# Performance work log

Hardware: AMD Instinct MI355X
Metric: run time of the kernel (lower is better)

The kernel has to match this reference:

```python
import jax, jax.numpy as jnp
import numpy as np

T, DIM, HID = 8192, 1024, 4096

def setup_inputs() -> dict:
    key = jax.random.key(0)
    k1, k2, k3 = jax.random.split(key, 3)
    x = jax.random.normal(k1, (T, DIM), dtype=jnp.float32)
    # torch Linear weight layout: [out_features, in_features]
    W_fc = jax.random.normal(k2, (HID, DIM), dtype=jnp.float32) * 0.02
    W_proj = jax.random.normal(k3, (DIM, HID), dtype=jnp.float32) * 0.02
    return {"x": x, "W_fc": W_fc, "W_proj": W_proj}

def reference(x, W_fc, W_proj):
    # fc: x @ W_fc^T  -> relu -> square -> proj: @ W_proj^T
    h = jnp.einsum('td,hd->th', x, W_fc)      # [T, HID]
    h = jnp.square(jax.nn.relu(h))            # relu(h)^2 (relu^2 activation)
    return jnp.einsum('th,dh->td', h, W_proj) # [T, DIM]
```

## Files before the change

### kernel.cpp

```cpp
#include <hip/hip_runtime.h>
#include <stdint.h>


typedef __attribute__((ext_vector_type(8))) short bf16x8;
typedef __attribute__((ext_vector_type(4))) float f32x4;

typedef const __attribute__((address_space(1))) unsigned int* gas_u32p;
typedef __attribute__((address_space(3))) unsigned int* las_u32p;

__device__ __forceinline__ void load16_to_lds(const void* gptr, void* lptr) {
    __builtin_amdgcn_global_load_lds((gas_u32p)gptr, (las_u32p)lptr, 16, 0, 0);
}

__device__ __forceinline__ unsigned short f2bf(float f) {
    unsigned int u = __float_as_uint(f);
    u += 0x7FFFu + ((u >> 16) & 1u);
    return (unsigned short)(u >> 16);
}

__global__ void cvt_all(const float4* __restrict__ x,  ushort4* __restrict__ xb,
                        const float4* __restrict__ wf, ushort4* __restrict__ wfb,
                        const float4* __restrict__ wp, ushort4* __restrict__ wpb)
{
    const int base = blockIdx.x * 1024 + threadIdx.x;
    #pragma unroll
    for (int j = 0; j < 4; j++) {
        const int i = base + j * 256;
        const float4* s; ushort4* d; int k;
        if (i < (1 << 21))            { s = x;  d = xb;  k = i; }
        else if (i < 3 * (1 << 20))   { s = wf; d = wfb; k = i - (1 << 21); }
        else                          { s = wp; d = wpb; k = i - 3 * (1 << 20); }
        float4 v = s[k];
        ushort4 o;
        o.x = f2bf(v.x); o.y = f2bf(v.y); o.z = f2bf(v.z); o.w = f2bf(v.w);
        d[k] = o;
    }
}

#define LGKM0_FENCE() do { \
    asm volatile("s_waitcnt lgkmcnt(0)" ::: "memory"); \
    __builtin_amdgcn_sched_barrier(0); } while (0)

template<int NF, bool RELU2, bool OUT_BF16>
__global__ __launch_bounds__(512, 2)
void gemm8p(const unsigned short* __restrict__ A,
            const unsigned short* __restrict__ B,
            void* __restrict__ Cv, int M, int N, int K)
{
    constexpr int BM   = 256;
    constexpr int BN   = 64 * NF;
    constexpr int CB   = BN / 128;
    constexpr int AKH  = 16384;
    constexpr int BKH  = BN * 64;
    constexpr int BOFF = 2 * AKH;
    constexpr int BUFB = 2 * AKH + 2 * BKH;
    constexpr int KEEP = 2 + 2 * CB;
    (void)M;

    __shared__ char lds[2 * BUFB];

    const int tid  = threadIdx.x;
    const int lane = tid & 63;
    const int wave = tid >> 6;
    const int wm   = wave >> 2;
    const int wn   = wave & 3;
    const int quad = lane >> 4;
    const int m16  = lane & 15;

    const int gx = gridDim.x;
    int flat = blockIdx.y * gx + blockIdx.x;
    const int cpx = (gx * gridDim.y) >> 3;
    flat = (flat & 7) * cpx + (flat >> 3);
    const long bm0 = (long)(flat / gx) * BM;
    const long bn0 = (long)(flat % gx) * BN;

    const int srow   = tid >> 2;
    const int schunk = (tid & 3) ^ ((tid >> 3) & 3);
    const unsigned short* gA = A + (bm0 + srow) * (long)K + schunk * 8;
    const unsigned short* gB = B + (bn0 + srow) * (long)K + schunk * 8;
    char* lbase = (char*)lds;

    int offA[8], offB[NF];
    #pragma unroll
    for (int i = 0; i < 8; i++) {
        const int lo = (wm * 128 + i * 16 + m16) * 64 + quad * 16;
        offA[i] = lo ^ (((lo >> 7) & 3) << 4);
    }
    #pragma unroll
    for (int j = 0; j < NF; j++) {
        const int lo = (wn * 16 * NF + j * 16 + m16) * 64 + quad * 16;
        offB[j] = lo ^ (((lo >> 7) & 3) << 4);
    }

    f32x4 acc[8][NF];
    #pragma unroll
    for (int i = 0; i < 8; i++)
        #pragma unroll
        for (int j = 0; j < NF; j++)
            acc[i][j] = (f32x4)0.0f;

    const int NT = K >> 6;

    #define STAGE_A(t, kh) do { \
        char* _d = lbase + ((t) & 1) * BUFB + (kh) * AKH + tid * 16; \
        const unsigned short* _s = gA + (long)(t) * 64 + (kh) * 32; \
        load16_to_lds(_s, _d); \
        load16_to_lds(_s + 128l * K, _d + 8192); } while (0)

    #define STAGE_B(t, kh) do { \
        char* _d = lbase + ((t) & 1) * BUFB + BOFF + (kh) * BKH + tid * 16; \
        const unsigned short* _s = gB + (long)(t) * 64 + (kh) * 32; \
        load16_to_lds(_s, _d); \
        if (CB == 2) load16_to_lds(_s + 128l * K, _d + 8192); } while (0)

    STAGE_B(0, 0); STAGE_A(0, 0); STAGE_B(0, 1); STAGE_A(0, 1);
    if (NT > 1) {
        STAGE_B(1, 0); STAGE_A(1, 0); STAGE_B(1, 1);
        asm volatile("s_waitcnt vmcnt(%0)" :: "i"(KEEP) : "memory");
    } else {
        asm volatile("s_waitcnt vmcnt(0)" ::: "memory");
    }
    __builtin_amdgcn_sched_barrier(0);
    __builtin_amdgcn_s_barrier();

    for (int t = 0; t < NT; ++t) {
        char* bufA = lbase + (t & 1) * BUFB;
        char* bufB = bufA + BOFF;
        bf16x8 af[4], bf[NF];

        #pragma unroll
        for (int j = 0; j < NF; j++) bf[j] = *(const bf16x8*)(bufB + offB[j]);
        #pragma unroll
        for (int i = 0; i < 4; i++)  af[i] = *(const bf16x8*)(bufA + offA[i]);
        if (t + 1 < NT) STAGE_A(t + 1, 1);
        __builtin_amdgcn_s_barrier();
        LGKM0_FENCE();
        __builtin_amdgcn_s_setprio(1);
        #pragma unroll
        for (int i = 0; i < 4; i++)
            #pragma unroll
            for (int j = 0; j < NF; j++)
                acc[i][j] = __builtin_amdgcn_mfma_f32_16x16x32_bf16(
                    af[i], bf[j], acc[i][j], 0, 0, 0);
        __builtin_amdgcn_s_setprio(0);
        __builtin_amdgcn_s_barrier();

        #pragma unroll
        for (int i = 0; i < 4; i++)  af[i] = *(const bf16x8*)(bufA + offA[4 + i]);
        if (t + 2 < NT) STAGE_B(t + 2, 0);
        __builtin_amdgcn_s_barrier();
        LGKM0_FENCE();
        __builtin_amdgcn_s_setprio(1);
        #pragma unroll
        for (int i = 0; i < 4; i++)
            #pragma unroll
            for (int j = 0; j < NF; j++)
                acc[4 + i][j] = __builtin_amdgcn_mfma_f32_16x16x32_bf16(
                    af[i], bf[j], acc[4 + i][j], 0, 0, 0);
        __builtin_amdgcn_s_setprio(0);
        __builtin_amdgcn_s_barrier();

        #pragma unroll
        for (int j = 0; j < NF; j++) bf[j] = *(const bf16x8*)(bufB + BKH + offB[j]);
        #pragma unroll
        for (int i = 0; i < 4; i++)  af[i] = *(const bf16x8*)(bufA + AKH + offA[i]);
        if (t + 2 < NT) STAGE_A(t + 2, 0);
        __builtin_amdgcn_s_barrier();
        LGKM0_FENCE();
        __builtin_amdgcn_s_setprio(1);
        #pragma unroll
        for (int i = 0; i < 4; i++)
            #pragma unroll
            for (int j = 0; j < NF; j++)
                acc[i][j] = __builtin_amdgcn_mfma_f32_16x16x32_bf16(
                    af[i], bf[j], acc[i][j], 0, 0, 0);
        __builtin_amdgcn_s_setprio(0);
        __builtin_amdgcn_s_barrier();

        #pragma unroll
        for (int i = 0; i < 4; i++)  af[i] = *(const bf16x8*)(bufA + AKH + offA[4 + i]);
        if (t + 2 < NT) STAGE_B(t + 2, 1);
        __builtin_amdgcn_s_barrier();
        LGKM0_FENCE();
        __builtin_amdgcn_s_setprio(1);
        #pragma unroll
        for (int i = 0; i < 4; i++)
            #pragma unroll
            for (int j = 0; j < NF; j++)
                acc[4 + i][j] = __builtin_amdgcn_mfma_f32_16x16x32_bf16(
                    af[i], bf[j], acc[4 + i][j], 0, 0, 0);
        __builtin_amdgcn_s_setprio(0);
        if (t + 2 < NT) asm volatile("s_waitcnt vmcnt(%0)" :: "i"(KEEP) : "memory");
        else            asm volatile("s_waitcnt vmcnt(0)" ::: "memory");
        __builtin_amdgcn_sched_barrier(0);
        __builtin_amdgcn_s_barrier();
    }
    #undef STAGE_A
    #undef STAGE_B

    const long baseRow = bm0 + wm * 128 + quad * 4;
    const long baseCol = bn0 + wn * 16 * NF + m16;
    #pragma unroll
    for (int i = 0; i < 8; i++) {
        #pragma unroll
        for (int j = 0; j < NF; j++) {
            #pragma unroll
            for (int r = 0; r < 4; r++) {
                float v = acc[i][j][r];
                if (RELU2) v = (v > 0.0f) ? v * v : 0.0f;
                const long row = baseRow + i * 16 + r;
                const long col = baseCol + j * 16;
                if (OUT_BF16)
                    ((unsigned short*)Cv)[row * (long)N + col] = f2bf(v);
                else
                    ((float*)Cv)[row * (long)N + col] = v;
            }
        }
    }
}

extern "C" void kernel_launch(void* const* d_in, const int* in_sizes, int n_in,
                              void* d_out, int out_size, void* d_ws, size_t ws_size,
                              hipStream_t stream) {
    (void)in_sizes; (void)n_in; (void)out_size; (void)ws_size;

    const int T = 8192, DIM = 1024, HID = 4096;

    const float* x     = (const float*)d_in[0];
    const float* W_fc  = (const float*)d_in[1];
    const float* W_prj = (const float*)d_in[2];
    float* out = (float*)d_out;

    char* ws = (char*)d_ws;
    unsigned short* h   = (unsigned short*)ws;
    unsigned short* xb  = (unsigned short*)(ws + (64l << 20));
    unsigned short* wfb = (unsigned short*)(ws + (80l << 20));
    unsigned short* wpb = (unsigned short*)(ws + (88l << 20));

    cvt_all<<<4096, 256, 0, stream>>>(
        (const float4*)x,     (ushort4*)xb,
        (const float4*)W_fc,  (ushort4*)wfb,
        (const float4*)W_prj, (ushort4*)wpb);

    gemm8p<4, true, true><<<dim3(HID / 256, T / 256), dim3(512), 0, stream>>>(
        xb, wfb, h, T, HID, DIM);

    gemm8p<2, false, false><<<dim3(DIM / 128, T / 256), dim3(512), 0, stream>>>(
        h, wpb, out, T, DIM, HID);
}
```

Baseline: 244.9 us.

## Add skewed half-K pipelined GEMM kernel for projection with XCD-aware block remap

Replaces the second GEMM (h @ W_proj^T) with a new kernel that splits each 64-wide K tile into two halves, issuing async global-to-LDS loads for later halves while MFMAs run on earlier ones, with explicit waitcnt, barriers and setprio control. Block indices are remapped across 8 groups so that neighbouring tiles land on the same XCD. LDS reads use inline ds_read_b128 with XOR swizzle. It aims to hide load latency and improve L2 locality, at the cost of hand-tuned wait counts that are fragile and tied to the K tiling.

```diff
diff --git a/kernel.cpp b/kernel.cpp
--- a/kernel.cpp
+++ b/kernel.cpp
@@ -10,6 +10,10 @@
 
 __device__ __forceinline__ void load16_to_lds(const void* gptr, void* lptr) {
     __builtin_amdgcn_global_load_lds((gas_u32p)gptr, (las_u32p)lptr, 16, 0, 0);
+}
+
+__device__ __forceinline__ void dsr128(bf16x8& d, unsigned off) {
+    asm volatile("ds_read_b128 %0, %1" : "=v"(d) : "v"(off));
 }
 
 __device__ __forceinline__ unsigned short f2bf(float f) {
@@ -219,6 +223,141 @@
     }
 }
 
+__global__ __launch_bounds__(512, 2)
+void gemm_skew(const unsigned short* __restrict__ A,
+               const unsigned short* __restrict__ B,
+               float* __restrict__ C, int M, int N, int K)
+{
+    constexpr int AKH  = 16384;
+    constexpr int BKH  = 8192;
+    constexpr int BOFF = 2 * AKH;
+    constexpr int BUFB = 2 * AKH + 2 * BKH;
+    (void)M;
+
+    __shared__ char lds[2 * BUFB];
+
+    const int tid  = threadIdx.x;
+    const int lane = tid & 63;
+    const int wave = tid >> 6;
+    const int wm   = wave >> 1;
+    const int wn   = wave & 1;
+    const int quad = lane >> 4;
+    const int m16  = lane & 15;
+
+    const int gx = gridDim.x;
+    int flat = blockIdx.y * gx + blockIdx.x;
+    const int cpx = (gx * gridDim.y) >> 3;
+    flat = (flat & 7) * cpx + (flat >> 3);
+    const long bm0 = (long)(flat / gx) * 256;
+    const long bn0 = (long)(flat % gx) * 128;
+
+    const int srow   = tid >> 2;
+    const int schunk = (tid & 3) ^ ((tid >> 3) & 3);
+    const unsigned short* gA = A + (bm0 + srow) * (long)K + schunk * 8;
+    const unsigned short* gB = B + (bn0 + srow) * (long)K + schunk * 8;
+
+    unsigned offA[4], offB[4];
+    #pragma unroll
+    for (int i = 0; i < 4; i++) {
+        const unsigned lo = (unsigned)((wm * 64 + i * 16 + m16) * 64 + quad * 16);
+        offA[i] = lo ^ (((lo >> 7) & 3) << 4);
+    }
+    #pragma unroll
+    for (int j = 0; j < 4; j++) {
+        const unsigned lo = (unsigned)((wn * 64 + j * 16 + m16) * 64 + quad * 16);
+        offB[j] = lo ^ (((lo >> 7) & 3) << 4);
+    }
+
+    const unsigned ldsbase =
+        (unsigned)(unsigned long long)(las_u32p)(void*)lds;
+
+    f32x4 acc[4][4];
+    #pragma unroll
+    for (int i = 0; i < 4; i++)
+        #pragma unroll
+        for (int j = 0; j < 4; j++)
+            acc[i][j] = (f32x4)0.0f;
+
+    const int NT = K >> 6;
+
+    #define STAGE2(t, kh) do { \
+        char* _dA = (char*)lds + ((t) & 1) * BUFB + (kh) * AKH + tid * 16; \
+        const unsigned short* _sA = gA + (long)(t) * 64 + (kh) * 32; \
+        load16_to_lds(_sA, _dA); \
+        load16_to_lds(_sA + 128l * K, _dA + 8192); \
+        char* _dB = (char*)lds + ((t) & 1) * BUFB + BOFF + (kh) * BKH + tid * 16; \
+        load16_to_lds(gB + (long)(t) * 64 + (kh) * 32, _dB); } while (0)
+
+    STAGE2(0, 0); STAGE2(0, 1);
+    if (NT > 1) {
+        STAGE2(1, 0);
+        asm volatile("s_waitcnt vmcnt(3)" ::: "memory");
+    } else {
+        asm volatile("s_waitcnt vmcnt(0)" ::: "memory");
+    }
+    __builtin_amdgcn_sched_barrier(0);
+    __builtin_amdgcn_s_barrier();
+
+    for (int t = 0; t < NT; ++t) {
+        const unsigned bufo = ldsbase + (unsigned)((t & 1) * BUFB);
+        bf16x8 a0[4], b0[4], a1[4], b1[4];
+
+        #pragma unroll
+        for (int i = 0; i < 4; i++) dsr128(a0[i], bufo + offA[i]);
+        #pragma unroll
+        for (int j = 0; j < 4; j++) dsr128(b0[j], bufo + BOFF + offB[j]);
+        #pragma unroll
+        for (int i = 0; i < 4; i++) dsr128(a1[i], bufo + AKH + offA[i]);
+        #pragma unroll
+        for (int j = 0; j < 4; j++) dsr128(b1[j], bufo + BOFF + BKH + offB[j]);
+        if (t + 1 < NT) STAGE2(t + 1, 1);
+        __builtin_amdgcn_s_barrier();
+        asm volatile("s_waitcnt lgkmcnt(8)" ::: "memory");
+        __builtin_amdgcn_sched_barrier(0);
+        __builtin_amdgcn_s_setprio(1);
+        #pragma unroll
+        for (int i = 0; i < 4; i++)
+            #pragma unroll
+            for (int j = 0; j < 4; j++)
+                acc[i][j] = __builtin_amdgcn_mfma_f32_16x16x32_bf16(
+                    a0[i], b0[j], acc[i][j], 0, 0, 0);
+        __builtin_amdgcn_s_setprio(0);
+        __builtin_amdgcn_s_barrier();
+
+        if (t + 2 < NT) STAGE2(t + 2, 0);
+        asm volatile("s_waitcnt lgkmcnt(0)" ::: "memory");
+        __builtin_amdgcn_sched_barrier(0);
+        __builtin_amdgcn_s_setprio(1);
+        #pragma unroll
+        for (int i = 0; i < 4; i++)
+            #pragma unroll
+            for (int j = 0; j < 4; j++)
+                acc[i][j] = __builtin_amdgcn_mfma_f32_16x16x32_bf16(
+                    a1[i], b1[j], acc[i][j], 0, 0, 0);
+        __builtin_amdgcn_s_setprio(0);
+        if (t + 2 < NT) asm volatile("s_waitcnt vmcnt(3)" ::: "memory");
+        else            asm volatile("s_waitcnt vmcnt(0)" ::: "memory");
+        __builtin_amdgcn_sched_barrier(0);
+        __builtin_amdgcn_s_barrier();
+    }
+    #undef STAGE2
+
+    const long baseRow = bm0 + wm * 64 + quad * 4;
+    const long baseCol = bn0 + wn * 64 + m16;
+    #pragma unroll
+    for (int i = 0; i < 4; i++) {
+        #pragma unroll
+        for (int j = 0; j < 4; j++) {
+            #pragma unroll
+            for (int r = 0; r < 4; r++) {
+                const long row = baseRow + i * 16 + r;
+                const long col = baseCol + j * 16;
+                C[row * (long)N + col] = acc[i][j][r];
+            }
+        }
+    }
+}
+
 extern "C" void kernel_launch(void* const* d_in, const int* in_sizes, int n_in,
                               void* d_out, int out_size, void* d_ws, size_t ws_size,
                               hipStream_t stream) {
@@ -245,6 +384,6 @@
     gemm8p<4, true, true><<<dim3(HID / 256, T / 256), dim3(512), 0, stream>>>(
         xb, wfb, h, T, HID, DIM);
 
-    gemm8p<2, false, false><<<dim3(DIM / 128, T / 256), dim3(512), 0, stream>>>(
+    gemm_skew<<<dim3(DIM / 128, T / 256), dim3(512), 0, stream>>>(
         h, wpb, out, T, DIM, HID);
 }
```

Result: no change. 242.6 us (-0.9%).
